# Performance work log

Measured on AMD Instinct MI355X. Metric: run time of the kernel, lower is better.

Reference implementation:

```python
import jax, jax.numpy as jnp
import numpy as np

B, P, NB, WN, CI, CO = 4, 20000, 9, 17, 64, 128

def setup_inputs() -> dict:
    key = jax.random.key(0)
    k0, k1, k2, k3 = jax.random.split(key, 4)
    in_pc = jax.random.normal(k0, (B, P, CI), dtype=jnp.float32)
    raw_w_weights = jax.random.normal(k1, (P, NB, WN), dtype=jnp.float32) * 0.1
    # padded/missing neighbors use id == P, which indexes the zero-pad row and is masked
    neighbor_ids = jax.random.randint(k2, (P, NB), 0, P + 1)
    weights = jax.random.normal(k3, (WN, CO * CI), dtype=jnp.float32)
    bias = jnp.zeros((P, CO), dtype=jnp.float32)
    return {"in_pc": in_pc, "raw_w_weights": raw_w_weights, "weights": weights,
            "bias": bias, "neighbor_ids": neighbor_ids}

def reference(in_pc, raw_w_weights, weights, bias, neighbor_ids):
    b, p, ci = in_pc.shape
    wn = weights.shape[0]
    co = bias.shape[-1]
    # pc_mask: 1 for real points, 0 for the pad row (id == in_pn)
    nb_mask = (neighbor_ids < p).astype(in_pc.dtype)          # [p, nb]
    w_weights = raw_w_weights * nb_mask[:, :, None]           # [p, nb, wn]
    in_pc_pad = jnp.concatenate(
        [in_pc, jnp.zeros((b, 1, ci), dtype=in_pc.dtype)], axis=1)  # [b, p+1, ci]
    in_neighbors = in_pc_pad[:, neighbor_ids]                 # [b, p, nb, ci] gather
    # weighted fuse over neighbors into wn basis slots
    fuse = jnp.einsum('pnm,bpni->bpmi', w_weights, in_neighbors)   # [b, p, wn, ci]
    Wm = weights.reshape(wn, co, ci)
    # per-basis conv then sum-reduce over wn (b_max_pool=False), fused into one einsum
    out_pc = jnp.einsum('moi,bpmi->bpo', Wm, fuse) + bias      # [b, p, co]
    # is_final_layer=False -> ELU; residual_rate=0 -> no residual branch
    return jax.nn.elu(out_pc)
```

## Files before the change

kernel.cpp:

```cpp
#include <hip/hip_runtime.h>
#include <stdint.h>

#define B_   4
#define P_   20000
#define NB_  9
#define WN_  17
#define CI_  64
#define CO_  128
#define PTS  16
#define NBLK (P_ / PTS)

typedef __fp16 f16x8 __attribute__((ext_vector_type(8)));
typedef __fp16 h2    __attribute__((ext_vector_type(2)));
typedef float  f32x16 __attribute__((ext_vector_type(16)));

union H2U { h2 h; uint32_t u; };
union F8U { f16x8 v; h2 h[4]; uint4 u; };

__global__ void prep_wm(const float* __restrict__ w, ushort* __restrict__ wsb) {
    int i = blockIdx.x * 256 + threadIdx.x;
    int m2p  = i >> 9;
    int r    = i & 511;
    int oloc = r >> 7, co = r & 127;
    int m = m2p >> 1, p = m2p & 1;
    const float* src = w + (size_t)m * (CO_ * CI_) + co * CI_ + (p * 4 + oloc) * 8;
    float4 v0 = *(const float4*)(src);
    float4 v1 = *(const float4*)(src + 4);
    F8U h;
    h.h[0] = __builtin_amdgcn_cvt_pkrtz(v0.x, v0.y);
    h.h[1] = __builtin_amdgcn_cvt_pkrtz(v0.z, v0.w);
    h.h[2] = __builtin_amdgcn_cvt_pkrtz(v1.x, v1.y);
    h.h[3] = __builtin_amdgcn_cvt_pkrtz(v1.z, v1.w);
    *(uint4*)&wsb[(size_t)((m2p * 4 + oloc) * 128 + co) * 8] = h.u;
}

template <bool PRE>
__global__ __launch_bounds__(256, 3)
void lasm_fused(const float* __restrict__ in_pc,
                const float* __restrict__ raw_w,
                const float* __restrict__ weights,
                const float* __restrict__ bias,
                const int*   __restrict__ nbr,
                const ushort* __restrict__ wsb,
                float*       __restrict__ out)
{
    __shared__ __align__(16) int      s_nid[PTS * NB_];
    __shared__ __align__(16) uint32_t s_w2[WN_ * NB_ * 17];

    const int tid  = threadIdx.x;
    const int lane = tid & 63;
    const int wv   = tid >> 6;
    const int arow = lane & 31;
    const int q    = lane >> 5;
    const int mt   = wv >> 1;
    const int ch   = wv & 1;
    const int p0   = blockIdx.x * PTS;

    if (tid < PTS * NB_) s_nid[tid] = nbr[p0 * NB_ + tid];
    for (int idx = tid; idx < PTS * NB_ * WN_; idx += 256) {
        int pl2 = idx / (NB_ * WN_);
        int rem = idx % (NB_ * WN_);
        int n   = rem / WN_;
        int m   = rem % WN_;
        float wf = raw_w[(size_t)p0 * NB_ * WN_ + idx];
        H2U c; c.h = __builtin_amdgcn_cvt_pkrtz(wf, wf);
        s_w2[(m * NB_ + n) * 17 + pl2] = c.u;
    }
    __syncthreads();

    f32x16 acc[2];
    #pragma unroll
    for (int c = 0; c < 2; ++c)
        #pragma unroll
        for (int j = 0; j < 16; ++j) acc[c][j] = 0.f;

    const int brow = mt * 2 + (arow >> 4);
    const int pl   = arow & 15;
    const size_t binpc = (size_t)brow * P_ * CI_;

    auto load_b = [&](int m, int pass, int kk, int c) -> f16x8 {
        int oloc = kk * 2 + q;
        if (PRE) {
            F8U r;
            r.u = *(const uint4*)&wsb[(size_t)(((m * 2 + pass) * 4 + oloc) * 128
                                               + ch * 64 + c * 32 + arow) * 8];
            return r.v;
        } else {
            const float* s = weights + (size_t)m * (CO_ * CI_)
                           + (ch * 64 + c * 32 + arow) * CI_ + (pass * 4 + oloc) * 8;
            float4 v0 = *(const float4*)(s);
            float4 v1 = *(const float4*)(s + 4);
            F8U r;
            r.h[0] = __builtin_amdgcn_cvt_pkrtz(v0.x, v0.y);
            r.h[1] = __builtin_amdgcn_cvt_pkrtz(v0.z, v0.w);
            r.h[2] = __builtin_amdgcn_cvt_pkrtz(v1.x, v1.y);
            r.h[3] = __builtin_amdgcn_cvt_pkrtz(v1.z, v1.w);
            return r.v;
        }
    };

    for (int pass = 0; pass < 2; ++pass) {
        h2 x[NB_][8];
        const int ch0 = pass * 32 + q * 8;
        #pragma unroll
        for (int n = 0; n < NB_; ++n) {
            uint32_t nid = (uint32_t)s_nid[pl * NB_ + n];
            if (nid < (uint32_t)P_) {
                const float* src = in_pc + binpc + (size_t)nid * CI_ + ch0;
                float4 a0 = *(const float4*)(src);
                float4 a1 = *(const float4*)(src + 4);
                float4 b0 = *(const float4*)(src + 16);
                float4 b1 = *(const float4*)(src + 20);
                x[n][0] = __builtin_amdgcn_cvt_pkrtz(a0.x, a0.y);
                x[n][1] = __builtin_amdgcn_cvt_pkrtz(a0.z, a0.w);
                x[n][2] = __builtin_amdgcn_cvt_pkrtz(a1.x, a1.y);
                x[n][3] = __builtin_amdgcn_cvt_pkrtz(a1.z, a1.w);
                x[n][4] = __builtin_amdgcn_cvt_pkrtz(b0.x, b0.y);
                x[n][5] = __builtin_amdgcn_cvt_pkrtz(b0.z, b0.w);
                x[n][6] = __builtin_amdgcn_cvt_pkrtz(b1.x, b1.y);
                x[n][7] = __builtin_amdgcn_cvt_pkrtz(b1.z, b1.w);
            } else {
                h2 z = {(__fp16)0.f, (__fp16)0.f};
                #pragma unroll
                for (int j = 0; j < 8; ++j) x[n][j] = z;
            }
        }

        f16x8 bA0 = load_b(0, pass, 0, 0);
        f16x8 bA1 = load_b(0, pass, 0, 1);

        for (int m = 0; m < WN_; ++m) {
            H2U wc[9];
            #pragma unroll
            for (int n = 0; n < NB_; ++n) wc[n].u = s_w2[(m * NB_ + n) * 17 + pl];

            F8U f[2];
            #pragma unroll
            for (int kk = 0; kk < 2; ++kk) {
                #pragma unroll
                for (int r4 = 0; r4 < 4; ++r4) {
                    h2 c = {(__fp16)0.f, (__fp16)0.f};
                    #pragma unroll
                    for (int n = 0; n < NB_; ++n) c += wc[n].h * x[n][kk * 4 + r4];
                    f[kk].h[r4] = c;
                }
            }

            f16x8 bB0 = load_b(m, pass, 1, 0);
            f16x8 bB1 = load_b(m, pass, 1, 1);
            acc[0] = __builtin_amdgcn_mfma_f32_32x32x16_f16(f[0].v, bA0, acc[0], 0, 0, 0);
            acc[1] = __builtin_amdgcn_mfma_f32_32x32x16_f16(f[0].v, bA1, acc[1], 0, 0, 0);

            int mn = (m + 1 < WN_) ? m + 1 : m;
            f16x8 nA0 = load_b(mn, pass, 0, 0);
            f16x8 nA1 = load_b(mn, pass, 0, 1);
            acc[0] = __builtin_amdgcn_mfma_f32_32x32x16_f16(f[1].v, bB0, acc[0], 0, 0, 0);
            acc[1] = __builtin_amdgcn_mfma_f32_32x32x16_f16(f[1].v, bB1, acc[1], 0, 0, 0);
            bA0 = nA0; bA1 = nA1;
        }
    }

    #pragma unroll
    for (int c = 0; c < 2; ++c) {
        int col = ch * 64 + c * 32 + arow;
        #pragma unroll
        for (int v = 0; v < 16; ++v) {
            int lr = (v & 3) + 8 * (v >> 2) + 4 * q;
            int b  = mt * 2 + (lr >> 4);
            int p  = p0 + (lr & 15);
            float val = acc[c][v] + bias[(size_t)p * CO_ + col];
            val = (val > 0.f) ? val : (__expf(val) - 1.f);
            __builtin_nontemporal_store(val, &out[((size_t)b * P_ + p) * CO_ + col]);
        }
    }
}

extern "C" void kernel_launch(void* const* d_in, const int* in_sizes, int n_in,
                              void* d_out, int out_size, void* d_ws, size_t ws_size,
                              hipStream_t stream) {
    const float* in_pc   = (const float*)d_in[0];
    const float* raw_w   = (const float*)d_in[1];
    const float* weights = (const float*)d_in[2];
    const float* bias    = (const float*)d_in[3];
    const int*   nbr     = (const int*)  d_in[4];
    float* out = (float*)d_out;

    const size_t need = (size_t)WN_ * 2 * 4096 * sizeof(ushort);
    if (d_ws != nullptr && ws_size >= need) {
        ushort* wsb = (ushort*)d_ws;
        prep_wm<<<dim3(WN_ * 2 * 512 / 256), dim3(256), 0, stream>>>(weights, wsb);
        lasm_fused<true><<<dim3(NBLK), dim3(256), 0, stream>>>(
            in_pc, raw_w, weights, bias, nbr, wsb, out);
    } else {
        lasm_fused<false><<<dim3(NBLK), dim3(256), 0, stream>>>(
            in_pc, raw_w, weights, bias, nbr, nullptr, out);
    }
}
```

Baseline: 164.1 us.

## Split channel passes into four to cut register pressure and raise occupancy

The K dimension of the per-basis MFMA is now processed in four passes of 16 input channels instead of two passes of 32, so each thread holds half as many gathered neighbor values and fused fragments. The weight prep layout is simplified to one octet-major layout per basis, and launch bounds are raised from 3 to 4 blocks per CU. The aim is lower VGPR use and more waves in flight to hide gather latency. In exchange the neighbor gather is issued twice as often in smaller pieces, and the per-basis weight loads and loop overhead double.

```diff
diff --git a/kernel.cpp b/kernel.cpp
--- a/kernel.cpp
+++ b/kernel.cpp
@@ -19,11 +19,10 @@
 
 __global__ void prep_wm(const float* __restrict__ w, ushort* __restrict__ wsb) {
     int i = blockIdx.x * 256 + threadIdx.x;
-    int m2p  = i >> 9;
-    int r    = i & 511;
-    int oloc = r >> 7, co = r & 127;
-    int m = m2p >> 1, p = m2p & 1;
-    const float* src = w + (size_t)m * (CO_ * CI_) + co * CI_ + (p * 4 + oloc) * 8;
+    int m   = i >> 10;
+    int r   = i & 1023;
+    int oct = r >> 7, co = r & 127;
+    const float* src = w + (size_t)m * (CO_ * CI_) + co * CI_ + oct * 8;
     float4 v0 = *(const float4*)(src);
     float4 v1 = *(const float4*)(src + 4);
     F8U h;
@@ -31,11 +30,11 @@
     h.h[1] = __builtin_amdgcn_cvt_pkrtz(v0.z, v0.w);
     h.h[2] = __builtin_amdgcn_cvt_pkrtz(v1.x, v1.y);
     h.h[3] = __builtin_amdgcn_cvt_pkrtz(v1.z, v1.w);
-    *(uint4*)&wsb[(size_t)((m2p * 4 + oloc) * 128 + co) * 8] = h.u;
+    *(uint4*)&wsb[(size_t)((m * 8 + oct) * 128 + co) * 8] = h.u;
 }
 
 template <bool PRE>
-__global__ __launch_bounds__(256, 3)
+__global__ __launch_bounds__(256, 4)
 void lasm_fused(const float* __restrict__ in_pc,
                 const float* __restrict__ raw_w,
                 const float* __restrict__ weights,
@@ -77,17 +76,18 @@
     const int brow = mt * 2 + (arow >> 4);
     const int pl   = arow & 15;
     const size_t binpc = (size_t)brow * P_ * CI_;
+    const int oct =  q;
 
-    auto load_b = [&](int m, int pass, int kk, int c) -> f16x8 {
-        int oloc = kk * 2 + q;
+    auto load_b = [&](int m, int pass, int c) -> f16x8 {
+        int o = 2 * pass + q;
         if (PRE) {
             F8U r;
-            r.u = *(const uint4*)&wsb[(size_t)(((m * 2 + pass) * 4 + oloc) * 128
+            r.u = *(const uint4*)&wsb[(size_t)((m * 8 + o) * 128
                                                + ch * 64 + c * 32 + arow) * 8];
             return r.v;
         } else {
             const float* s = weights + (size_t)m * (CO_ * CI_)
-                           + (ch * 64 + c * 32 + arow) * CI_ + (pass * 4 + oloc) * 8;
+                           + (ch * 64 + c * 32 + arow) * CI_ + o * 8;
             float4 v0 = *(const float4*)(s);
             float4 v1 = *(const float4*)(s + 4);
             F8U r;
@@ -99,9 +99,10 @@
         }
     };
 
-    for (int pass = 0; pass < 2; ++pass) {
-        h2 x[NB_][8];
-        const int ch0 = pass * 32 + q * 8;
+    #pragma unroll 1
+    for (int pass = 0; pass < 4; ++pass) {
+        h2 x[NB_][4];
+        const int ch0 = (2 * pass + q) * 8;
         #pragma unroll
         for (int n = 0; n < NB_; ++n) {
             uint32_t nid = (uint32_t)s_nid[pl * NB_ + n];
@@ -109,54 +110,39 @@
                 const float* src = in_pc + binpc + (size_t)nid * CI_ + ch0;
                 float4 a0 = *(const float4*)(src);
                 float4 a1 = *(const float4*)(src + 4);
-                float4 b0 = *(const float4*)(src + 16);
-                float4 b1 = *(const float4*)(src + 20);
                 x[n][0] = __builtin_amdgcn_cvt_pkrtz(a0.x, a0.y);
                 x[n][1] = __builtin_amdgcn_cvt_pkrtz(a0.z, a0.w);
                 x[n][2] = __builtin_amdgcn_cvt_pkrtz(a1.x, a1.y);
                 x[n][3] = __builtin_amdgcn_cvt_pkrtz(a1.z, a1.w);
-                x[n][4] = __builtin_amdgcn_cvt_pkrtz(b0.x, b0.y);
-                x[n][5] = __builtin_amdgcn_cvt_pkrtz(b0.z, b0.w);
-                x[n][6] = __builtin_amdgcn_cvt_pkrtz(b1.x, b1.y);
-                x[n][7] = __builtin_amdgcn_cvt_pkrtz(b1.z, b1.w);
             } else {
                 h2 z = {(__fp16)0.f, (__fp16)0.f};
-                #pragma unroll
-                for (int j = 0; j < 8; ++j) x[n][j] = z;
+                x[n][0] = z; x[n][1] = z; x[n][2] = z; x[n][3] = z;
             }
         }
 
-        f16x8 bA0 = load_b(0, pass, 0, 0);
-        f16x8 bA1 = load_b(0, pass, 0, 1);
+        f16x8 bC0 = load_b(0, pass, 0);
+        f16x8 bC1 = load_b(0, pass, 1);
 
         for (int m = 0; m < WN_; ++m) {
             H2U wc[9];
             #pragma unroll
             for (int n = 0; n < NB_; ++n) wc[n].u = s_w2[(m * NB_ + n) * 17 + pl];
 
-            F8U f[2];
+            F8U f;
             #pragma unroll
-            for (int kk = 0; kk < 2; ++kk) {
+            for (int r4 = 0; r4 < 4; ++r4) {
+                h2 c = {(__fp16)0.f, (__fp16)0.f};
                 #pragma unroll
-                for (int r4 = 0; r4 < 4; ++r4) {
-                    h2 c = {(__fp16)0.f, (__fp16)0.f};
-                    #pragma unroll
-                    for (int n = 0; n < NB_; ++n) c += wc[n].h * x[n][kk * 4 + r4];
-                    f[kk].h[r4] = c;
-                }
+                for (int n = 0; n < NB_; ++n) c += wc[n].h * x[n][r4];
+                f.h[r4] = c;
             }
 
-            f16x8 bB0 = load_b(m, pass, 1, 0);
-            f16x8 bB1 = load_b(m, pass, 1, 1);
-            acc[0] = __builtin_amdgcn_mfma_f32_32x32x16_f16(f[0].v, bA0, acc[0], 0, 0, 0);
-            acc[1] = __builtin_amdgcn_mfma_f32_32x32x16_f16(f[0].v, bA1, acc[1], 0, 0, 0);
-
             int mn = (m + 1 < WN_) ? m + 1 : m;
-            f16x8 nA0 = load_b(mn, pass, 0, 0);
-            f16x8 nA1 = load_b(mn, pass, 0, 1);
-            acc[0] = __builtin_amdgcn_mfma_f32_32x32x16_f16(f[1].v, bB0, acc[0], 0, 0, 0);
-            acc[1] = __builtin_amdgcn_mfma_f32_32x32x16_f16(f[1].v, bB1, acc[1], 0, 0, 0);
-            bA0 = nA0; bA1 = nA1;
+            f16x8 n0 = load_b(mn, pass, 0);
+            f16x8 n1 = load_b(mn, pass, 1);
+            acc[0] = __builtin_amdgcn_mfma_f32_32x32x16_f16(f.v, bC0, acc[0], 0, 0, 0);
+            acc[1] = __builtin_amdgcn_mfma_f32_32x32x16_f16(f.v, bC1, acc[1], 0, 0, 0);
+            bC0 = n0; bC1 = n1;
         }
     }
 
@@ -185,10 +171,10 @@
     const int*   nbr     = (const int*)  d_in[4];
     float* out = (float*)d_out;
 
-    const size_t need = (size_t)WN_ * 2 * 4096 * sizeof(ushort);
+    const size_t need = (size_t)WN_ * 8 * 128 * 8 * sizeof(ushort);
     if (d_ws != nullptr && ws_size >= need) {
         ushort* wsb = (ushort*)d_ws;
-        prep_wm<<<dim3(WN_ * 2 * 512 / 256), dim3(256), 0, stream>>>(weights, wsb);
+        prep_wm<<<dim3(WN_ * 1024 / 256), dim3(256), 0, stream>>>(weights, wsb);
         lasm_fused<true><<<dim3(NBLK), dim3(256), 0, stream>>>(
             in_pc, raw_w, weights, bias, nbr, wsb, out);
     } else {
```

New measurement: 500.4 us. +205.0%, slower.
